# Kernel tuning notes

Measured on AMD Instinct MI355X. Metric: run time of the kernel, lower is better.

The kernel has to match this reference:

```python
import jax, jax.numpy as jnp
import numpy as np

B, S, E, H = 2, 2048, 1024, 16
DK = E // H


def setup_inputs() -> dict:
    key = jax.random.key(0)
    ks = jax.random.split(key, 11)
    std = 1.0 / np.sqrt(E)
    inp = {
        "q": jax.random.normal(ks[0], (B, S, E), jnp.float32),
        "k": jax.random.normal(ks[1], (B, S, E), jnp.float32),
        "v": jax.random.normal(ks[2], (B, S, E), jnp.float32),
        # causal mask, broadcast over batch and heads; scores with mask==0 get -1e9
        "mask": jnp.tril(jnp.ones((S, S), jnp.int32))[None, None],
        # torch nn.Linear weights: [out_features, in_features]
        "w_q": jax.random.normal(ks[3], (E, E), jnp.float32) * std,
        "b_q": jax.random.normal(ks[4], (E,), jnp.float32) * std,
        "w_k": jax.random.normal(ks[5], (E, E), jnp.float32) * std,
        "b_k": jax.random.normal(ks[6], (E,), jnp.float32) * std,
        "w_v": jax.random.normal(ks[7], (E, E), jnp.float32) * std,
        "b_v": jax.random.normal(ks[8], (E,), jnp.float32) * std,
        "w_o": jax.random.normal(ks[9], (E, E), jnp.float32) * std,
        "b_o": jax.random.normal(ks[10], (E,), jnp.float32) * std,
    }
    return inp


def reference(q, k, v, mask, w_q, b_q, w_k, b_k, w_v, b_v, w_o, b_o):
    # linear projections (torch Linear: x @ W.T + b)
    query = q @ w_q.T + b_q
    key = k @ w_k.T + b_k
    value = v @ w_v.T + b_v
    # [B, S, E] -> [B, H, S, DK]
    query = query.reshape(B, S, H, DK).transpose(0, 2, 1, 3)
    key = key.reshape(B, S, H, DK).transpose(0, 2, 1, 3)
    value = value.reshape(B, S, H, DK).transpose(0, 2, 1, 3)
    scale = 1.0 / jnp.sqrt(jnp.asarray(DK, query.dtype))
    scores = jnp.einsum("bhqd,bhkd->bhqk", query, key) * scale
    scores = jnp.where(mask == 0, jnp.asarray(-1e9, scores.dtype), scores)
    attn = jax.nn.softmax(scores, axis=-1)  # dropout p=0.0 -> identity
    x = jnp.einsum("bhqk,bhkd->bhqd", attn, value)
    x = x.transpose(0, 2, 1, 3).reshape(B, S, E)
    return x @ w_o.T + b_o
```

## Files before the change

kernel.cpp:

```cpp
#include <hip/hip_runtime.h>
#include <stdint.h>

typedef __attribute__((ext_vector_type(8))) short short8;
typedef __attribute__((ext_vector_type(4))) float f32x4;
typedef unsigned short u16;

#define SEQ 2048
#define EMB 1024
#define NH 16
#define DK 64
#define MTOT 4096
#define CEXP 0.18033688011112042f

__device__ __forceinline__ u16 f2bf(float f) {
  union { float f; unsigned int u; } x; x.f = f;
  unsigned int r = x.u + 0x7fffu + ((x.u >> 16) & 1u);
  return (u16)(r >> 16);
}

__device__ __forceinline__ void gload_lds16(const void* g, void* l) {
  __builtin_amdgcn_global_load_lds(
      (const __attribute__((address_space(1))) unsigned int*)g,
      (__attribute__((address_space(3))) unsigned int*)l,
      16, 0, 0);
}

__global__ __launch_bounds__(256) void cvt3(const float* __restrict__ a,
                                            const float* __restrict__ b,
                                            const float* __restrict__ c,
                                            u16* __restrict__ d) {
  const float* s = (blockIdx.y == 0) ? a : ((blockIdx.y == 1) ? b : c);
  size_t base = (size_t)blockIdx.y * (MTOT * (size_t)EMB / 4);
  int i = blockIdx.x * 256 + threadIdx.x;
  float4 v = ((const float4*)s)[i];
  ushort4 o;
  o.x = f2bf(v.x); o.y = f2bf(v.y); o.z = f2bf(v.z); o.w = f2bf(v.w);
  ((ushort4*)d)[base + i] = o;
}

__global__ __launch_bounds__(256) void cvt4(const float* __restrict__ a,
                                            const float* __restrict__ b,
                                            const float* __restrict__ c,
                                            const float* __restrict__ e,
                                            u16* __restrict__ d) {
  const float* s = (blockIdx.y == 0) ? a
                 : ((blockIdx.y == 1) ? b : ((blockIdx.y == 2) ? c : e));
  size_t base = (size_t)blockIdx.y * ((size_t)EMB * EMB / 4);
  int i = blockIdx.x * 256 + threadIdx.x;
  float4 v = ((const float4*)s)[i];
  ushort4 o;
  o.x = f2bf(v.x); o.y = f2bf(v.y); o.z = f2bf(v.z); o.w = f2bf(v.w);
  ((ushort4*)d)[base + i] = o;
}

template <int MODE>
__device__ __forceinline__ void gemm_core(const u16* __restrict__ A,
                                          const u16* __restrict__ W,
                                          const float* __restrict__ bias,
                                          void* __restrict__ dst,
                                          int m0, int n0,
                                          u16* As, u16* Bs) {
  const int K = EMB;
  int tid = threadIdx.x, lane = tid & 63, wid = tid >> 6;
  int g = lane >> 4, l15 = lane & 15;
  int wr = wid >> 1, wc = wid & 1;

  f32x4 acc[4][4];
#pragma unroll
  for (int mi = 0; mi < 4; ++mi)
#pragma unroll
    for (int ni = 0; ni < 4; ++ni) acc[mi][ni] = (f32x4)(0.0f);

  for (int kt = 0; kt < K / 64; ++kt) {
    int k0 = kt * 64;
#pragma unroll
    for (int i = 0; i < 4; ++i) {
      int off = (wid * 4 + i) * 1024;
      int elem = (off >> 1) + lane * 8;
      int row = elem >> 6, col = elem & 63;
      gload_lds16(A + (size_t)(m0 + row) * K + k0 + col, (char*)As + off);
      gload_lds16(W + (size_t)(n0 + row) * K + k0 + col, (char*)Bs + off);
    }
    __syncthreads();
#pragma unroll
    for (int kk = 0; kk < 2; ++kk) {
      short8 af[4], bf[4];
#pragma unroll
      for (int mi = 0; mi < 4; ++mi)
        af[mi] = *(const short8*)&As[(wr * 64 + mi * 16 + l15) * 64 + kk * 32 + 8 * g];
#pragma unroll
      for (int ni = 0; ni < 4; ++ni)
        bf[ni] = *(const short8*)&Bs[(wc * 64 + ni * 16 + l15) * 64 + kk * 32 + 8 * g];
#pragma unroll
      for (int mi = 0; mi < 4; ++mi)
#pragma unroll
        for (int ni = 0; ni < 4; ++ni)
          acc[mi][ni] = __builtin_amdgcn_mfma_f32_16x16x32_bf16(af[mi], bf[ni],
                                                                acc[mi][ni], 0, 0, 0);
    }
    __syncthreads();
  }

#pragma unroll
  for (int ni = 0; ni < 4; ++ni) {
    int n_g = n0 + wc * 64 + ni * 16 + l15;
    float bv = bias[n_g];
#pragma unroll
    for (int mi = 0; mi < 4; ++mi) {
#pragma unroll
      for (int j = 0; j < 4; ++j) {
        int m_g = m0 + wr * 64 + mi * 16 + 4 * g + j;
        float v = acc[mi][ni][j] + bv;
        if (MODE == 0) {
          int b = m_g >> 11, s = m_g & (SEQ - 1);
          int h = n_g >> 6, d = n_g & 63;
          ((u16*)dst)[((((size_t)b * NH + h) * SEQ + s) << 6) + d] = f2bf(v);
        } else {
          ((float*)dst)[(size_t)m_g * EMB + n_g] = v;
        }
      }
    }
  }
}

__global__ __launch_bounds__(256, 2) void gemm_qkv(const u16* __restrict__ Aall,
                                                   const u16* __restrict__ Wall,
                                                   const float* __restrict__ bq,
                                                   const float* __restrict__ bk,
                                                   const float* __restrict__ bv,
                                                   u16* __restrict__ QKVh) {
  __shared__ __align__(16) u16 As[128 * 64];
  __shared__ __align__(16) u16 Bs[128 * 64];
  int bl = blockIdx.x;
  int xcd = bl & 7, i = bl >> 3;
  int bx = i & 7;
  int j = i >> 3;
  int z = j >> 2;
  int by = xcd * 4 + (j & 3);
  const u16* A = Aall + (size_t)z * MTOT * EMB;
  const u16* W = Wall + (size_t)z * EMB * EMB;
  const float* bias = (z == 0) ? bq : ((z == 1) ? bk : bv);
  u16* dst = QKVh + (size_t)z * MTOT * EMB;
  gemm_core<0>(A, W, bias, dst, by * 128, bx * 128, As, Bs);
}

__global__ __launch_bounds__(256, 2) void gemm_out(const u16* __restrict__ X,
                                                   const u16* __restrict__ Wo,
                                                   const float* __restrict__ bo,
                                                   float* __restrict__ out) {
  __shared__ __align__(16) u16 As[128 * 64];
  __shared__ __align__(16) u16 Bs[128 * 64];
  int bl = blockIdx.x;
  int xcd = bl & 7, i = bl >> 3;
  int bx = i & 7;
  int by = xcd * 4 + (i >> 3);
  gemm_core<1>(X, Wo, bo, out, by * 128, bx * 128, As, Bs);
}

__global__ __launch_bounds__(256, 4) void flash_attn(const u16* __restrict__ Qh,
                                                     const u16* __restrict__ Kh,
                                                     const u16* __restrict__ Vh,
                                                     u16* __restrict__ X) {
  __shared__ __align__(16) u16 Ks[2][64][64];
  __shared__ __align__(16) u16 Vt[2][64][64];

  int tid = threadIdx.x, lane = tid & 63, wid = tid >> 6;
  int g = lane >> 4, l15 = lane & 15;

  int bl = blockIdx.x;
  int xcd = bl & 7, idx = bl >> 3;
  int c = idx & 31, r = idx >> 5;
  int bh = xcd * 4 + r;
  int cc = (r >= 2) ? ((c + 16) & 31) : c;
  int qt = (r & 1) ? (31 - cc) : cc;

  int q0 = qt * 64, qw = q0 + wid * 16;
  int qrow = qw + l15;

  const short8* qp = (const short8*)(Qh + ((size_t)bh * SEQ + qrow) * DK + 8 * g);
  short8 fq0 = qp[0], fq1 = qp[4];

  int kvbase = 8 * (l15 >> 2) + (l15 & 3);
  int ksw = ((l15 & 3) | (((l15 >> 2) & 1) << 2)) << 3;
  int vsw = (l15 & 7) << 3;
  const u16* Kb = Kh + (size_t)bh * SEQ * DK;
  const u16* Vb = Vh + (size_t)bh * SEQ * DK;

  int krow_st = wid * 16 + (lane >> 3);
  int kcol_st = (lane & 7) * 8;

  f32x4 sc[4], oacc[4];
#pragma unroll
  for (int i = 0; i < 4; ++i) oacc[i] = (f32x4)(0.0f);
  float m_run = -1e30f, l_part = 0.0f;

#pragma unroll
  for (int i = 0; i < 2; ++i) {
    int rw = krow_st + i * 8;
    int wsw = (((rw & 3) | (((rw >> 3) & 1) << 2)) << 3);
    short8 kt = *(const short8*)(Kb + (size_t)rw * DK + kcol_st);
    *(short8*)(&Ks[0][0][0] + rw * 64 + (kcol_st ^ wsw)) = kt;
  }
#pragma unroll
  for (int it2 = 0; it2 < 2; ++it2) {
    int kvb = wid * 8 + it2 * 32;
    short8 tmp;
#pragma unroll
    for (int i = 0; i < 8; ++i)
      tmp[i] = (short)Vb[(size_t)(kvb + i) * DK + lane];
    *(short8*)(&Vt[0][0][0] + lane * 64 + (kvb ^ ((lane & 7) << 3))) = tmp;
  }
  __syncthreads();

  for (int t = 0; t <= qt; ++t) {
    int kv0 = t * 64;
    int cur = t & 1;

    short8 ktmp[2];
    u16 vtmp[16];
    if (t < qt) {
      int kvn = kv0 + 64;
#pragma unroll
      for (int i = 0; i < 2; ++i)
        ktmp[i] = *(const short8*)(Kb + (size_t)(kvn + krow_st + i * 8) * DK + kcol_st);
#pragma unroll
      for (int it2 = 0; it2 < 2; ++it2)
#pragma unroll
        for (int i = 0; i < 8; ++i)
          vtmp[it2 * 8 + i] = Vb[(size_t)(kvn + wid * 8 + it2 * 32 + i) * DK + lane];
    }

    {
      const u16* base = &Ks[cur][0][0];
      short8 kf[4][2];
#pragma unroll
      for (int cq = 0; cq < 4; ++cq) {
        int krow = kvbase + 4 * (cq & 1) + 32 * (cq >> 1);
        kf[cq][0] = *(const short8*)(base + krow * 64 + ((8 * g) ^ ksw));
        kf[cq][1] = *(const short8*)(base + krow * 64 + ((8 * g + 32) ^ ksw));
      }
      __builtin_amdgcn_s_setprio(1);
#pragma unroll
      for (int cq = 0; cq < 4; ++cq) {
        f32x4 z = (f32x4)(0.0f);
        z = __builtin_amdgcn_mfma_f32_16x16x32_bf16(kf[cq][0], fq0, z, 0, 0, 0);
        z = __builtin_amdgcn_mfma_f32_16x16x32_bf16(kf[cq][1], fq1, z, 0, 0, 0);
        sc[cq] = z;
      }
      __builtin_amdgcn_s_setprio(0);
    }

    if (t == qt) {
#pragma unroll
      for (int cq = 0; cq < 4; ++cq) {
        int kvc = kv0 + 8 * g + 4 * (cq & 1) + 32 * (cq >> 1);
#pragma unroll
        for (int j = 0; j < 4; ++j)
          if (kvc + j > qrow) sc[cq][j] = -1e30f;
      }
    }

    float vmax = sc[0][0];
#pragma unroll
    for (int cq = 0; cq < 4; ++cq)
#pragma unroll
      for (int j = 0; j < 4; ++j) vmax = fmaxf(vmax, sc[cq][j]);
    vmax = fmaxf(vmax, __shfl_xor(vmax, 16));
    vmax = fmaxf(vmax, __shfl_xor(vmax, 32));

    if (!__all(vmax - m_run <= 44.0f)) {
      float mnew = fmaxf(m_run, vmax);
      float alpha = exp2f((m_run - mnew) * CEXP);
      l_part *= alpha;
#pragma unroll
      for (int c2 = 0; c2 < 4; ++c2)
#pragma unroll
        for (int j = 0; j < 4; ++j) oacc[c2][j] *= alpha;
      m_run = mnew;
    }

#pragma unroll
    for (int cq = 0; cq < 4; ++cq)
#pragma unroll
      for (int j = 0; j < 4; ++j) {
        float p = exp2f((sc[cq][j] - m_run) * CEXP);
        sc[cq][j] = p;
        l_part += p;
      }

    union { short8 s8; uint32_t w[4]; } pa[2];
#pragma unroll
    for (int h = 0; h < 2; ++h)
#pragma unroll
      for (int i = 0; i < 4; ++i) {
        float lo = sc[2 * h + (i >> 1)][(i & 1) * 2];
        float hi = sc[2 * h + (i >> 1)][(i & 1) * 2 + 1];
        asm("v_cvt_pk_bf16_f32 %0, %1, %2" : "=v"(pa[h].w[i]) : "v"(lo), "v"(hi));
      }

    __builtin_amdgcn_s_setprio(1);
#pragma unroll
    for (int c2 = 0; c2 < 4; ++c2)
#pragma unroll
      for (int h = 0; h < 2; ++h) {
        short8 av = *(const short8*)(&Vt[cur][0][0] + (c2 * 16 + l15) * 64 +
                                     ((h * 32 + 8 * g) ^ vsw));
        oacc[c2] = __builtin_amdgcn_mfma_f32_16x16x32_bf16(av, pa[h].s8,
                                                           oacc[c2], 0, 0, 0);
      }
    __builtin_amdgcn_s_setprio(0);

    if (t < qt) {
#pragma unroll
      for (int i = 0; i < 2; ++i) {
        int rw = krow_st + i * 8;
        int wsw = (((rw & 3) | (((rw >> 3) & 1) << 2)) << 3);
        *(short8*)(&Ks[cur ^ 1][0][0] + rw * 64 + (kcol_st ^ wsw)) = ktmp[i];
      }
#pragma unroll
      for (int it2 = 0; it2 < 2; ++it2) {
        short8 w;
#pragma unroll
        for (int i = 0; i < 8; ++i) w[i] = (short)vtmp[it2 * 8 + i];
        int kvb = wid * 8 + it2 * 32;
        *(short8*)(&Vt[cur ^ 1][0][0] + lane * 64 + (kvb ^ ((lane & 7) << 3))) = w;
      }
    }
    __syncthreads();
  }

  float ls = l_part;
  ls += __shfl_xor(ls, 16);
  ls += __shfl_xor(ls, 32);
  float inv = 1.0f / ls;
  u16* ow = &Vt[0][0][0] + wid * 16 * 64;
#pragma unroll
  for (int c2 = 0; c2 < 4; ++c2)
#pragma unroll
    for (int jp = 0; jp < 2; ++jp) {
      float lo = oacc[c2][2 * jp] * inv, hi = oacc[c2][2 * jp + 1] * inv;
      uint32_t w;
      asm("v_cvt_pk_bf16_f32 %0, %1, %2" : "=v"(w) : "v"(lo), "v"(hi));
      *(uint32_t*)&ow[l15 * 64 + c2 * 16 + 4 * g + 2 * jp] = w;
    }
  __syncthreads();
  int rr = lane >> 2, dc = (lane & 3) * 16;
  short8 o0 = *(const short8*)&ow[rr * 64 + dc];
  short8 o1 = *(const short8*)&ow[rr * 64 + dc + 8];
  int b = bh >> 4, hh = bh & 15;
  size_t xo = ((size_t)b * SEQ + qw + rr) * EMB + hh * 64 + dc;
  *(short8*)&X[xo] = o0;
  *(short8*)&X[xo + 8] = o1;
}

extern "C" void kernel_launch(void* const* d_in, const int* in_sizes, int n_in,
                              void* d_out, int out_size, void* d_ws, size_t ws_size,
                              hipStream_t stream) {
  const float* q  = (const float*)d_in[0];
  const float* k  = (const float*)d_in[1];
  const float* v  = (const float*)d_in[2];
  const float* wq = (const float*)d_in[4];
  const float* bq = (const float*)d_in[5];
  const float* wk = (const float*)d_in[6];
  const float* bk = (const float*)d_in[7];
  const float* wv = (const float*)d_in[8];
  const float* bv = (const float*)d_in[9];
  const float* wo = (const float*)d_in[10];
  const float* bo = (const float*)d_in[11];

  u16* Aall = (u16*)d_ws;
  u16* Wall = Aall + (size_t)3 * MTOT * EMB;
  u16* QKVh = Wall + (size_t)4 * EMB * EMB;
  u16* Xb   = QKVh + (size_t)3 * MTOT * EMB;

  cvt3<<<dim3(MTOT * EMB / 4 / 256, 3), 256, 0, stream>>>(q, k, v, Aall);
  cvt4<<<dim3(EMB * EMB / 4 / 256, 4), 256, 0, stream>>>(wq, wk, wv, wo, Wall);

  gemm_qkv<<<768, 256, 0, stream>>>(Aall, Wall, bq, bk, bv, QKVh);

  const u16* Qh = QKVh;
  const u16* Kh = QKVh + (size_t)MTOT * EMB;
  const u16* Vh = QKVh + (size_t)2 * MTOT * EMB;
  flash_attn<<<1024, 256, 0, stream>>>(Qh, Kh, Vh, Xb);

  gemm_out<<<256, 256, 0, stream>>>(Xb, Wall + (size_t)3 * EMB * EMB, bo, (float*)d_out);
}
```

Measured before the change: 125.9 us.

## Pair causal q-tiles per block and peel diagonal tile out of attention loop

```diff
diff --git a/kernel.cpp b/kernel.cpp
--- a/kernel.cpp
+++ b/kernel.cpp
@@ -169,16 +169,9 @@
 
   int bl = blockIdx.x;
   int xcd = bl & 7, idx = bl >> 3;
-  int c = idx & 31, r = idx >> 5;
-  int bh = xcd * 4 + r;
-  int cc = (r >= 2) ? ((c + 16) & 31) : c;
-  int qt = (r & 1) ? (31 - cc) : cc;
-
-  int q0 = qt * 64, qw = q0 + wid * 16;
-  int qrow = qw + l15;
-
-  const short8* qp = (const short8*)(Qh + ((size_t)bh * SEQ + qrow) * DK + 8 * g);
-  short8 fq0 = qp[0], fq1 = qp[4];
+  int bhl = idx >> 4;
+  int p = idx & 15;
+  int bh = xcd * 4 + bhl;
 
   int kvbase = 8 * (l15 >> 2) + (l15 & 3);
   int ksw = ((l15 & 3) | (((l15 >> 2) & 1) << 2)) << 3;
@@ -189,48 +182,152 @@
   int krow_st = wid * 16 + (lane >> 3);
   int kcol_st = (lane & 7) * 8;
 
-  f32x4 sc[4], oacc[4];
-#pragma unroll
-  for (int i = 0; i < 4; ++i) oacc[i] = (f32x4)(0.0f);
-  float m_run = -1e30f, l_part = 0.0f;
-
-#pragma unroll
-  for (int i = 0; i < 2; ++i) {
-    int rw = krow_st + i * 8;
-    int wsw = (((rw & 3) | (((rw >> 3) & 1) << 2)) << 3);
-    short8 kt = *(const short8*)(Kb + (size_t)rw * DK + kcol_st);
-    *(short8*)(&Ks[0][0][0] + rw * 64 + (kcol_st ^ wsw)) = kt;
-  }
-#pragma unroll
-  for (int it2 = 0; it2 < 2; ++it2) {
-    int kvb = wid * 8 + it2 * 32;
-    short8 tmp;
-#pragma unroll
-    for (int i = 0; i < 8; ++i)
-      tmp[i] = (short)Vb[(size_t)(kvb + i) * DK + lane];
-    *(short8*)(&Vt[0][0][0] + lane * 64 + (kvb ^ ((lane & 7) << 3))) = tmp;
-  }
-  __syncthreads();
-
-  for (int t = 0; t <= qt; ++t) {
-    int kv0 = t * 64;
-    int cur = t & 1;
-
-    short8 ktmp[2];
-    u16 vtmp[16];
-    if (t < qt) {
-      int kvn = kv0 + 64;
-#pragma unroll
-      for (int i = 0; i < 2; ++i)
-        ktmp[i] = *(const short8*)(Kb + (size_t)(kvn + krow_st + i * 8) * DK + kcol_st);
-#pragma unroll
-      for (int it2 = 0; it2 < 2; ++it2)
-#pragma unroll
-        for (int i = 0; i < 8; ++i)
-          vtmp[it2 * 8 + i] = Vb[(size_t)(kvn + wid * 8 + it2 * 32 + i) * DK + lane];
+  for (int half = 0; half < 2; ++half) {
+    int qt = half ? (31 - p) : p;
+    int qw = qt * 64 + wid * 16;
+    int qrow = qw + l15;
+
+    const short8* qp = (const short8*)(Qh + ((size_t)bh * SEQ + qrow) * DK + 8 * g);
+    short8 fq0 = qp[0], fq1 = qp[4];
+
+    f32x4 sc[4], oacc[4];
+#pragma unroll
+    for (int i = 0; i < 4; ++i) oacc[i] = (f32x4)(0.0f);
+    float m_run = -1e30f, l_part = 0.0f;
+
+    __syncthreads();
+
+#pragma unroll
+    for (int i = 0; i < 2; ++i) {
+      int rw = krow_st + i * 8;
+      int wsw = (((rw & 3) | (((rw >> 3) & 1) << 2)) << 3);
+      short8 kt = *(const short8*)(Kb + (size_t)rw * DK + kcol_st);
+      *(short8*)(&Ks[0][0][0] + rw * 64 + (kcol_st ^ wsw)) = kt;
+    }
+#pragma unroll
+    for (int it2 = 0; it2 < 2; ++it2) {
+      int kvb = wid * 8 + it2 * 32;
+      short8 tmp;
+#pragma unroll
+      for (int i = 0; i < 8; ++i)
+        tmp[i] = (short)Vb[(size_t)(kvb + i) * DK + lane];
+      *(short8*)(&Vt[0][0][0] + lane * 64 + (kvb ^ ((lane & 7) << 3))) = tmp;
+    }
+    __syncthreads();
+
+    for (int t = 0; t < qt; ++t) {
+      int kv0 = t * 64;
+      int cur = t & 1;
+
+      short8 ktmp[2];
+      u16 vtmp[16];
+      {
+        int kvn = kv0 + 64;
+#pragma unroll
+        for (int i = 0; i < 2; ++i)
+          ktmp[i] = *(const short8*)(Kb + (size_t)(kvn + krow_st + i * 8) * DK + kcol_st);
+#pragma unroll
+        for (int it2 = 0; it2 < 2; ++it2)
+#pragma unroll
+          for (int i = 0; i < 8; ++i)
+            vtmp[it2 * 8 + i] = Vb[(size_t)(kvn + wid * 8 + it2 * 32 + i) * DK + lane];
+      }
+
+      {
+        const u16* base = &Ks[cur][0][0];
+        short8 kf[4][2];
+#pragma unroll
+        for (int cq = 0; cq < 4; ++cq) {
+          int krow = kvbase + 4 * (cq & 1) + 32 * (cq >> 1);
+          kf[cq][0] = *(const short8*)(base + krow * 64 + ((8 * g) ^ ksw));
+          kf[cq][1] = *(const short8*)(base + krow * 64 + ((8 * g + 32) ^ ksw));
+        }
+        __builtin_amdgcn_s_setprio(1);
+#pragma unroll
+        for (int cq = 0; cq < 4; ++cq) {
+          f32x4 z = (f32x4)(0.0f);
+          z = __builtin_amdgcn_mfma_f32_16x16x32_bf16(kf[cq][0], fq0, z, 0, 0, 0);
+          z = __builtin_amdgcn_mfma_f32_16x16x32_bf16(kf[cq][1], fq1, z, 0, 0, 0);
+          sc[cq] = z;
+        }
+        __builtin_amdgcn_s_setprio(0);
+      }
+
+      float m01a = fmaxf(sc[0][0], sc[0][1]), m01b = fmaxf(sc[0][2], sc[0][3]);
+      float m23a = fmaxf(sc[1][0], sc[1][1]), m23b = fmaxf(sc[1][2], sc[1][3]);
+      float m45a = fmaxf(sc[2][0], sc[2][1]), m45b = fmaxf(sc[2][2], sc[2][3]);
+      float m67a = fmaxf(sc[3][0], sc[3][1]), m67b = fmaxf(sc[3][2], sc[3][3]);
+      float vmax = fmaxf(fmaxf(fmaxf(m01a, m01b), fmaxf(m23a, m23b)),
+                         fmaxf(fmaxf(m45a, m45b), fmaxf(m67a, m67b)));
+      vmax = fmaxf(vmax, __shfl_xor(vmax, 16));
+      vmax = fmaxf(vmax, __shfl_xor(vmax, 32));
+
+      if (!__all(vmax - m_run <= 44.0f)) {
+        float mnew = fmaxf(m_run, vmax);
+        float alpha = exp2f((m_run - mnew) * CEXP);
+        l_part *= alpha;
+#pragma unroll
+        for (int c2 = 0; c2 < 4; ++c2)
+#pragma unroll
+          for (int j = 0; j < 4; ++j) oacc[c2][j] *= alpha;
+        m_run = mnew;
+      }
+
+      float negm = -m_run * CEXP;
+      float ls0 = 0.f, ls1 = 0.f, ls2 = 0.f, ls3 = 0.f;
+#pragma unroll
+      for (int cq = 0; cq < 4; ++cq) {
+        float p0 = exp2f(fmaf(sc[cq][0], CEXP, negm));
+        float p1 = exp2f(fmaf(sc[cq][1], CEXP, negm));
+        float p2 = exp2f(fmaf(sc[cq][2], CEXP, negm));
+        float p3 = exp2f(fmaf(sc[cq][3], CEXP, negm));
+        sc[cq][0] = p0; sc[cq][1] = p1; sc[cq][2] = p2; sc[cq][3] = p3;
+        ls0 += p0; ls1 += p1; ls2 += p2; ls3 += p3;
+      }
+      l_part += (ls0 + ls1) + (ls2 + ls3);
+
+      union { short8 s8; uint32_t w[4]; } pa[2];
+#pragma unroll
+      for (int h = 0; h < 2; ++h)
+#pragma unroll
+        for (int i = 0; i < 4; ++i) {
+          float lo = sc[2 * h + (i >> 1)][(i & 1) * 2];
+          float hi = sc[2 * h + (i >> 1)][(i & 1) * 2 + 1];
+          asm("v_cvt_pk_bf16_f32 %0, %1, %2" : "=v"(pa[h].w[i]) : "v"(lo), "v"(hi));
+        }
+
+      __builtin_amdgcn_s_setprio(1);
+#pragma unroll
+      for (int c2 = 0; c2 < 4; ++c2)
+#pragma unroll
+        for (int h = 0; h < 2; ++h) {
+          short8 av = *(const short8*)(&Vt[cur][0][0] + (c2 * 16 + l15) * 64 +
+                                       ((h * 32 + 8 * g) ^ vsw));
+          oacc[c2] = __builtin_amdgcn_mfma_f32_16x16x32_bf16(av, pa[h].s8,
+                                                             oacc[c2], 0, 0, 0);
+        }
+      __builtin_amdgcn_s_setprio(0);
+
+#pragma unroll
+      for (int i = 0; i < 2; ++i) {
+        int rw = krow_st + i * 8;
+        int wsw = (((rw & 3) | (((rw >> 3) & 1) << 2)) << 3);
+        *(short8*)(&Ks[cur ^ 1][0][0] + rw * 64 + (kcol_st ^ wsw)) = ktmp[i];
+      }
+#pragma unroll
+      for (int it2 = 0; it2 < 2; ++it2) {
+        short8 w;
+#pragma unroll
+        for (int i = 0; i < 8; ++i) w[i] = (short)vtmp[it2 * 8 + i];
+        int kvb = wid * 8 + it2 * 32;
+        *(short8*)(&Vt[cur ^ 1][0][0] + lane * 64 + (kvb ^ ((lane & 7) << 3))) = w;
+      }
+      __syncthreads();
     }
 
     {
+      int kv0 = qt * 64;
+      int cur = qt & 1;
       const u16* base = &Ks[cur][0][0];
       short8 kf[4][2];
 #pragma unroll
@@ -248,9 +345,7 @@
         sc[cq] = z;
       }
       __builtin_amdgcn_s_setprio(0);
-    }
-
-    if (t == qt) {
+
 #pragma unroll
       for (int cq = 0; cq < 4; ++cq) {
         int kvc = kv0 + 8 * g + 4 * (cq & 1) + 32 * (cq >> 1);
@@ -258,99 +353,83 @@
         for (int j = 0; j < 4; ++j)
           if (kvc + j > qrow) sc[cq][j] = -1e30f;
       }
-    }
-
-    float vmax = sc[0][0];
-#pragma unroll
-    for (int cq = 0; cq < 4; ++cq)
-#pragma unroll
-      for (int j = 0; j < 4; ++j) vmax = fmaxf(vmax, sc[cq][j]);
-    vmax = fmaxf(vmax, __shfl_xor(vmax, 16));
-    vmax = fmaxf(vmax, __shfl_xor(vmax, 32));
-
-    if (!__all(vmax - m_run <= 44.0f)) {
-      float mnew = fmaxf(m_run, vmax);
-      float alpha = exp2f((m_run - mnew) * CEXP);
-      l_part *= alpha;
+
+      float vmax = sc[0][0];
+#pragma unroll
+      for (int cq = 0; cq < 4; ++cq)
+#pragma unroll
+        for (int j = 0; j < 4; ++j) vmax = fmaxf(vmax, sc[cq][j]);
+      vmax = fmaxf(vmax, __shfl_xor(vmax, 16));
+      vmax = fmaxf(vmax, __shfl_xor(vmax, 32));
+
+      if (!__all(vmax - m_run <= 44.0f)) {
+        float mnew = fmaxf(m_run, vmax);
+        float alpha = exp2f((m_run - mnew) * CEXP);
+        l_part *= alpha;
+#pragma unroll
+        for (int c2 = 0; c2 < 4; ++c2)
+#pragma unroll
+          for (int j = 0; j < 4; ++j) oacc[c2][j] *= alpha;
+        m_run = mnew;
+      }
+
+      float negm = -m_run * CEXP;
+#pragma unroll
+      for (int cq = 0; cq < 4; ++cq)
+#pragma unroll
+        for (int j = 0; j < 4; ++j) {
+          float pp = exp2f(fmaf(sc[cq][j], CEXP, negm));
+          sc[cq][j] = pp;
+          l_part += pp;
+        }
+
+      union { short8 s8; uint32_t w[4]; } pa[2];
+#pragma unroll
+      for (int h = 0; h < 2; ++h)
+#pragma unroll
+        for (int i = 0; i < 4; ++i) {
+          float lo = sc[2 * h + (i >> 1)][(i & 1) * 2];
+          float hi = sc[2 * h + (i >> 1)][(i & 1) * 2 + 1];
+          asm("v_cvt_pk_bf16_f32 %0, %1, %2" : "=v"(pa[h].w[i]) : "v"(lo), "v"(hi));
+        }
+
+      __builtin_amdgcn_s_setprio(1);
 #pragma unroll
       for (int c2 = 0; c2 < 4; ++c2)
 #pragma unroll
-        for (int j = 0; j < 4; ++j) oacc[c2][j] *= alpha;
-      m_run = mnew;
-    }
-
-#pragma unroll
-    for (int cq = 0; cq < 4; ++cq)
-#pragma unroll
-      for (int j = 0; j < 4; ++j) {
-        float p = exp2f((sc[cq][j] - m_run) * CEXP);
-        sc[cq][j] = p;
-        l_part += p;
-      }
-
-    union { short8 s8; uint32_t w[4]; } pa[2];
-#pragma unroll
-    for (int h = 0; h < 2; ++h)
-#pragma unroll
-      for (int i = 0; i < 4; ++i) {
-        float lo = sc[2 * h + (i >> 1)][(i & 1) * 2];
-        float hi = sc[2 * h + (i >> 1)][(i & 1) * 2 + 1];
-        asm("v_cvt_pk_bf16_f32 %0, %1, %2" : "=v"(pa[h].w[i]) : "v"(lo), "v"(hi));
-      }
-
-    __builtin_amdgcn_s_setprio(1);
+        for (int h = 0; h < 2; ++h) {
+          short8 av = *(const short8*)(&Vt[cur][0][0] + (c2 * 16 + l15) * 64 +
+                                       ((h * 32 + 8 * g) ^ vsw));
+          oacc[c2] = __builtin_amdgcn_mfma_f32_16x16x32_bf16(av, pa[h].s8,
+                                                             oacc[c2], 0, 0, 0);
+        }
+      __builtin_amdgcn_s_setprio(0);
+    }
+    __syncthreads();
+
+    float ls = l_part;
+    ls += __shfl_xor(ls, 16);
+    ls += __shfl_xor(ls, 32);
+    float inv = 1.0f / ls;
+    u16* ow = &Vt[0][0][0] + wid * 16 * 64;
 #pragma unroll
     for (int c2 = 0; c2 < 4; ++c2)
 #pragma unroll
-      for (int h = 0; h < 2; ++h) {
-        short8 av = *(const short8*)(&Vt[cur][0][0] + (c2 * 16 + l15) * 64 +
-                                     ((h * 32 + 8 * g) ^ vsw));
-        oacc[c2] = __builtin_amdgcn_mfma_f32_16x16x32_bf16(av, pa[h].s8,
-                                                           oacc[c2], 0, 0, 0);
-      }
-    __builtin_amdgcn_s_setprio(0);
-
-    if (t < qt) {
-#pragma unroll
-      for (int i = 0; i < 2; ++i) {
-        int rw = krow_st + i * 8;
-        int wsw = (((rw & 3) | (((rw >> 3) & 1) << 2)) << 3);
-        *(short8*)(&Ks[cur ^ 1][0][0] + rw * 64 + (kcol_st ^ wsw)) = ktmp[i];
-      }
-#pragma unroll
-      for (int it2 = 0; it2 < 2; ++it2) {
-        short8 w;
-#pragma unroll
-        for (int i = 0; i < 8; ++i) w[i] = (short)vtmp[it2 * 8 + i];
-        int kvb = wid * 8 + it2 * 32;
-        *(short8*)(&Vt[cur ^ 1][0][0] + lane * 64 + (kvb ^ ((lane & 7) << 3))) = w;
-      }
-    }
-    __syncthreads();
+      for (int jp = 0; jp < 2; ++jp) {
+        float lo = oacc[c2][2 * jp] * inv, hi = oacc[c2][2 * jp + 1] * inv;
+        uint32_t w;
+        asm("v_cvt_pk_bf16_f32 %0, %1, %2" : "=v"(w) : "v"(lo), "v"(hi));
+        *(uint32_t*)&ow[l15 * 64 + c2 * 16 + 4 * g + 2 * jp] = w;
+      }
+    __syncthreads();
+    int rr = lane >> 2, dc = (lane & 3) * 16;
+    short8 o0 = *(const short8*)&ow[rr * 64 + dc];
+    short8 o1 = *(const short8*)&ow[rr * 64 + dc + 8];
+    int b = bh >> 4, hh = bh & 15;
+    size_t xo = ((size_t)b * SEQ + qw + rr) * EMB + hh * 64 + dc;
+    *(short8*)&X[xo] = o0;
+    *(short8*)&X[xo + 8] = o1;
   }
-
-  float ls = l_part;
-  ls += __shfl_xor(ls, 16);
-  ls += __shfl_xor(ls, 32);
-  float inv = 1.0f / ls;
-  u16* ow = &Vt[0][0][0] + wid * 16 * 64;
-#pragma unroll
-  for (int c2 = 0; c2 < 4; ++c2)
-#pragma unroll
-    for (int jp = 0; jp < 2; ++jp) {
-      float lo = oacc[c2][2 * jp] * inv, hi = oacc[c2][2 * jp + 1] * inv;
-      uint32_t w;
-      asm("v_cvt_pk_bf16_f32 %0, %1, %2" : "=v"(w) : "v"(lo), "v"(hi));
-      *(uint32_t*)&ow[l15 * 64 + c2 * 16 + 4 * g + 2 * jp] = w;
-    }
-  __syncthreads();
-  int rr = lane >> 2, dc = (lane & 3) * 16;
-  short8 o0 = *(const short8*)&ow[rr * 64 + dc];
-  short8 o1 = *(const short8*)&ow[rr * 64 + dc + 8];
-  int b = bh >> 4, hh = bh & 15;
-  size_t xo = ((size_t)b * SEQ + qw + rr) * EMB + hh * 64 + dc;
-  *(short8*)&X[xo] = o0;
-  *(short8*)&X[xo + 8] = o1;
 }
 
 extern "C" void kernel_launch(void* const* d_in, const int* in_sizes, int n_in,
@@ -381,7 +460,7 @@
   const u16* Qh = QKVh;
   const u16* Kh = QKVh + (size_t)MTOT * EMB;
   const u16* Vh = QKVh + (size_t)2 * MTOT * EMB;
-  flash_attn<<<1024, 256, 0, stream>>>(Qh, Kh, Vh, Xb);
+  flash_attn<<<512, 256, 0, stream>>>(Qh, Kh, Vh, Xb);
 
   gemm_out<<<256, 256, 0, stream>>>(Xb, Wall + (size_t)3 * EMB * EMB, bo, (float*)d_out);
 }
```

Result: no change. 126.5 us (+0.5%).

## Widen flash-attention blocks to 128 query rows sharing K/V tiles

Applied to the files above, without the earlier changes.

```diff
diff --git a/kernel.cpp b/kernel.cpp
--- a/kernel.cpp
+++ b/kernel.cpp
@@ -157,7 +157,7 @@
   gemm_core<1>(X, Wo, bo, out, by * 128, bx * 128, As, Bs);
 }
 
-__global__ __launch_bounds__(256, 4) void flash_attn(const u16* __restrict__ Qh,
+__global__ __launch_bounds__(512, 4) void flash_attn(const u16* __restrict__ Qh,
                                                      const u16* __restrict__ Kh,
                                                      const u16* __restrict__ Vh,
                                                      u16* __restrict__ X) {
@@ -169,13 +169,14 @@
 
   int bl = blockIdx.x;
   int xcd = bl & 7, idx = bl >> 3;
-  int c = idx & 31, r = idx >> 5;
-  int bh = xcd * 4 + r;
-  int cc = (r >= 2) ? ((c + 16) & 31) : c;
-  int qt = (r & 1) ? (31 - cc) : cc;
-
-  int q0 = qt * 64, qw = q0 + wid * 16;
+  int bhl = idx & 3, u = idx >> 2;
+  int qb = (u < 8) ? u : 23 - u;
+  int bh = xcd * 4 + bhl;
+
+  int qw = qb * 128 + wid * 16;
   int qrow = qw + l15;
+  int td = 2 * qb + (wid >> 2);
+  int NT = 2 * qb + 2;
 
   const short8* qp = (const short8*)(Qh + ((size_t)bh * SEQ + qrow) * DK + 8 * g);
   short8 fq0 = qp[0], fq1 = qp[4];
@@ -186,7 +187,7 @@
   const u16* Kb = Kh + (size_t)bh * SEQ * DK;
   const u16* Vb = Vh + (size_t)bh * SEQ * DK;
 
-  int krow_st = wid * 16 + (lane >> 3);
+  int krow_st = wid * 8 + (lane >> 3);
   int kcol_st = (lane & 7) * 8;
 
   f32x4 sc[4], oacc[4];
@@ -194,137 +195,122 @@
   for (int i = 0; i < 4; ++i) oacc[i] = (f32x4)(0.0f);
   float m_run = -1e30f, l_part = 0.0f;
 
-#pragma unroll
-  for (int i = 0; i < 2; ++i) {
-    int rw = krow_st + i * 8;
-    int wsw = (((rw & 3) | (((rw >> 3) & 1) << 2)) << 3);
-    short8 kt = *(const short8*)(Kb + (size_t)rw * DK + kcol_st);
-    *(short8*)(&Ks[0][0][0] + rw * 64 + (kcol_st ^ wsw)) = kt;
-  }
-#pragma unroll
-  for (int it2 = 0; it2 < 2; ++it2) {
-    int kvb = wid * 8 + it2 * 32;
+  {
+    int wsw = (((krow_st & 3) | (((krow_st >> 3) & 1) << 2)) << 3);
+    short8 kt = *(const short8*)(Kb + (size_t)krow_st * DK + kcol_st);
+    *(short8*)(&Ks[0][0][0] + krow_st * 64 + (kcol_st ^ wsw)) = kt;
     short8 tmp;
 #pragma unroll
     for (int i = 0; i < 8; ++i)
-      tmp[i] = (short)Vb[(size_t)(kvb + i) * DK + lane];
-    *(short8*)(&Vt[0][0][0] + lane * 64 + (kvb ^ ((lane & 7) << 3))) = tmp;
+      tmp[i] = (short)Vb[(size_t)(wid * 8 + i) * DK + lane];
+    *(short8*)(&Vt[0][0][0] + lane * 64 + ((wid * 8) ^ ((lane & 7) << 3))) = tmp;
   }
   __syncthreads();
 
-  for (int t = 0; t <= qt; ++t) {
+  for (int t = 0; t < NT; ++t) {
     int kv0 = t * 64;
     int cur = t & 1;
 
-    short8 ktmp[2];
-    u16 vtmp[16];
-    if (t < qt) {
+    short8 ktmp;
+    u16 vtmp[8];
+    if (t < NT - 1) {
       int kvn = kv0 + 64;
-#pragma unroll
-      for (int i = 0; i < 2; ++i)
-        ktmp[i] = *(const short8*)(Kb + (size_t)(kvn + krow_st + i * 8) * DK + kcol_st);
-#pragma unroll
-      for (int it2 = 0; it2 < 2; ++it2)
-#pragma unroll
-        for (int i = 0; i < 8; ++i)
-          vtmp[it2 * 8 + i] = Vb[(size_t)(kvn + wid * 8 + it2 * 32 + i) * DK + lane];
-    }
-
-    {
-      const u16* base = &Ks[cur][0][0];
-      short8 kf[4][2];
-#pragma unroll
-      for (int cq = 0; cq < 4; ++cq) {
-        int krow = kvbase + 4 * (cq & 1) + 32 * (cq >> 1);
-        kf[cq][0] = *(const short8*)(base + krow * 64 + ((8 * g) ^ ksw));
-        kf[cq][1] = *(const short8*)(base + krow * 64 + ((8 * g + 32) ^ ksw));
+      ktmp = *(const short8*)(Kb + (size_t)(kvn + krow_st) * DK + kcol_st);
+#pragma unroll
+      for (int i = 0; i < 8; ++i)
+        vtmp[i] = Vb[(size_t)(kvn + wid * 8 + i) * DK + lane];
+    }
+
+    if (t <= td) {
+      {
+        const u16* base = &Ks[cur][0][0];
+        short8 kf[4][2];
+#pragma unroll
+        for (int cq = 0; cq < 4; ++cq) {
+          int krow = kvbase + 4 * (cq & 1) + 32 * (cq >> 1);
+          kf[cq][0] = *(const short8*)(base + krow * 64 + ((8 * g) ^ ksw));
+          kf[cq][1] = *(const short8*)(base + krow * 64 + ((8 * g + 32) ^ ksw));
+        }
+        __builtin_amdgcn_s_setprio(1);
+#pragma unroll
+        for (int cq = 0; cq < 4; ++cq) {
+          f32x4 z = (f32x4)(0.0f);
+          z = __builtin_amdgcn_mfma_f32_16x16x32_bf16(kf[cq][0], fq0, z, 0, 0, 0);
+          z = __builtin_amdgcn_mfma_f32_16x16x32_bf16(kf[cq][1], fq1, z, 0, 0, 0);
+          sc[cq] = z;
+        }
+        __builtin_amdgcn_s_setprio(0);
       }
+
+      if (t == td) {
+#pragma unroll
+        for (int cq = 0; cq < 4; ++cq) {
+          int kvc = kv0 + 8 * g + 4 * (cq & 1) + 32 * (cq >> 1);
+#pragma unroll
+          for (int j = 0; j < 4; ++j)
+            if (kvc + j > qrow) sc[cq][j] = -1e30f;
+        }
+      }
+
+      float vmax = sc[0][0];
+#pragma unroll
+      for (int cq = 0; cq < 4; ++cq)
+#pragma unroll
+        for (int j = 0; j < 4; ++j) vmax = fmaxf(vmax, sc[cq][j]);
+      vmax = fmaxf(vmax, __shfl_xor(vmax, 16));
+      vmax = fmaxf(vmax, __shfl_xor(vmax, 32));
+
+      if (!__all(vmax - m_run <= 44.0f)) {
+        float mnew = fmaxf(m_run, vmax);
+        float alpha = exp2f((m_run - mnew) * CEXP);
+        l_part *= alpha;
+#pragma unroll
+        for (int c2 = 0; c2 < 4; ++c2)
+#pragma unroll
+          for (int j = 0; j < 4; ++j) oacc[c2][j] *= alpha;
+        m_run = mnew;
+      }
+
+      float negm = -m_run * CEXP;
+#pragma unroll
+      for (int cq = 0; cq < 4; ++cq)
+#pragma unroll
+        for (int j = 0; j < 4; ++j) {
+          float p = exp2f(fmaf(sc[cq][j], CEXP, negm));
+          sc[cq][j] = p;
+          l_part += p;
+        }
+
+      union { short8 s8; uint32_t w[4]; } pa[2];
+#pragma unroll
+      for (int h = 0; h < 2; ++h)
+#pragma unroll
+        for (int i = 0; i < 4; ++i) {
+          float lo = sc[2 * h + (i >> 1)][(i & 1) * 2];
+          float hi = sc[2 * h + (i >> 1)][(i & 1) * 2 + 1];
+          asm("v_cvt_pk_bf16_f32 %0, %1, %2" : "=v"(pa[h].w[i]) : "v"(lo), "v"(hi));
+        }
+
       __builtin_amdgcn_s_setprio(1);
 #pragma unroll
-      for (int cq = 0; cq < 4; ++cq) {
-        f32x4 z = (f32x4)(0.0f);
-        z = __builtin_amdgcn_mfma_f32_16x16x32_bf16(kf[cq][0], fq0, z, 0, 0, 0);
-        z = __builtin_amdgcn_mfma_f32_16x16x32_bf16(kf[cq][1], fq1, z, 0, 0, 0);
-        sc[cq] = z;
-      }
+      for (int c2 = 0; c2 < 4; ++c2)
+#pragma unroll
+        for (int h = 0; h < 2; ++h) {
+          short8 av = *(const short8*)(&Vt[cur][0][0] + (c2 * 16 + l15) * 64 +
+                                       ((h * 32 + 8 * g) ^ vsw));
+          oacc[c2] = __builtin_amdgcn_mfma_f32_16x16x32_bf16(av, pa[h].s8,
+                                                             oacc[c2], 0, 0, 0);
+        }
       __builtin_amdgcn_s_setprio(0);
     }
 
-    if (t == qt) {
-#pragma unroll
-      for (int cq = 0; cq < 4; ++cq) {
-        int kvc = kv0 + 8 * g + 4 * (cq & 1) + 32 * (cq >> 1);
-#pragma unroll
-        for (int j = 0; j < 4; ++j)
-          if (kvc + j > qrow) sc[cq][j] = -1e30f;
-      }
-    }
-
-    float vmax = sc[0][0];
-#pragma unroll
-    for (int cq = 0; cq < 4; ++cq)
-#pragma unroll
-      for (int j = 0; j < 4; ++j) vmax = fmaxf(vmax, sc[cq][j]);
-    vmax = fmaxf(vmax, __shfl_xor(vmax, 16));
-    vmax = fmaxf(vmax, __shfl_xor(vmax, 32));
-
-    if (!__all(vmax - m_run <= 44.0f)) {
-      float mnew = fmaxf(m_run, vmax);
-      float alpha = exp2f((m_run - mnew) * CEXP);
-      l_part *= alpha;
-#pragma unroll
-      for (int c2 = 0; c2 < 4; ++c2)
-#pragma unroll
-        for (int j = 0; j < 4; ++j) oacc[c2][j] *= alpha;
-      m_run = mnew;
-    }
-
-#pragma unroll
-    for (int cq = 0; cq < 4; ++cq)
-#pragma unroll
-      for (int j = 0; j < 4; ++j) {
-        float p = exp2f((sc[cq][j] - m_run) * CEXP);
-        sc[cq][j] = p;
-        l_part += p;
-      }
-
-    union { short8 s8; uint32_t w[4]; } pa[2];
-#pragma unroll
-    for (int h = 0; h < 2; ++h)
-#pragma unroll
-      for (int i = 0; i < 4; ++i) {
-        float lo = sc[2 * h + (i >> 1)][(i & 1) * 2];
-        float hi = sc[2 * h + (i >> 1)][(i & 1) * 2 + 1];
-        asm("v_cvt_pk_bf16_f32 %0, %1, %2" : "=v"(pa[h].w[i]) : "v"(lo), "v"(hi));
-      }
-
-    __builtin_amdgcn_s_setprio(1);
-#pragma unroll
-    for (int c2 = 0; c2 < 4; ++c2)
-#pragma unroll
-      for (int h = 0; h < 2; ++h) {
-        short8 av = *(const short8*)(&Vt[cur][0][0] + (c2 * 16 + l15) * 64 +
-                                     ((h * 32 + 8 * g) ^ vsw));
-        oacc[c2] = __builtin_amdgcn_mfma_f32_16x16x32_bf16(av, pa[h].s8,
-                                                           oacc[c2], 0, 0, 0);
-      }
-    __builtin_amdgcn_s_setprio(0);
-
-    if (t < qt) {
-#pragma unroll
-      for (int i = 0; i < 2; ++i) {
-        int rw = krow_st + i * 8;
-        int wsw = (((rw & 3) | (((rw >> 3) & 1) << 2)) << 3);
-        *(short8*)(&Ks[cur ^ 1][0][0] + rw * 64 + (kcol_st ^ wsw)) = ktmp[i];
-      }
-#pragma unroll
-      for (int it2 = 0; it2 < 2; ++it2) {
-        short8 w;
-#pragma unroll
-        for (int i = 0; i < 8; ++i) w[i] = (short)vtmp[it2 * 8 + i];
-        int kvb = wid * 8 + it2 * 32;
-        *(short8*)(&Vt[cur ^ 1][0][0] + lane * 64 + (kvb ^ ((lane & 7) << 3))) = w;
-      }
+    if (t < NT - 1) {
+      int wsw = (((krow_st & 3) | (((krow_st >> 3) & 1) << 2)) << 3);
+      *(short8*)(&Ks[cur ^ 1][0][0] + krow_st * 64 + (kcol_st ^ wsw)) = ktmp;
+      short8 w;
+#pragma unroll
+      for (int i = 0; i < 8; ++i) w[i] = (short)vtmp[i];
+      *(short8*)(&Vt[cur ^ 1][0][0] + lane * 64 + ((wid * 8) ^ ((lane & 7) << 3))) = w;
     }
     __syncthreads();
   }
@@ -333,7 +319,7 @@
   ls += __shfl_xor(ls, 16);
   ls += __shfl_xor(ls, 32);
   float inv = 1.0f / ls;
-  u16* ow = &Vt[0][0][0] + wid * 16 * 64;
+  u16* ow = &Ks[0][0][0] + wid * 16 * 64;
 #pragma unroll
   for (int c2 = 0; c2 < 4; ++c2)
 #pragma unroll
@@ -381,7 +367,7 @@
   const u16* Qh = QKVh;
   const u16* Kh = QKVh + (size_t)MTOT * EMB;
   const u16* Vh = QKVh + (size_t)2 * MTOT * EMB;
-  flash_attn<<<1024, 256, 0, stream>>>(Qh, Kh, Vh, Xb);
+  flash_attn<<<512, 512, 0, stream>>>(Qh, Kh, Vh, Xb);
 
   gemm_out<<<256, 256, 0, stream>>>(Xb, Wall + (size_t)3 * EMB * EMB, bo, (float*)d_out);
 }
```

Result: slower. 130.1 us (+3.4%).

## Fuse fp32-to-bf16 activation conversion into QKV projection GEMM A-tile load

Applied to the files above, without the earlier changes.

```diff
diff --git a/kernel.cpp b/kernel.cpp
--- a/kernel.cpp
+++ b/kernel.cpp
@@ -25,24 +25,11 @@
       16, 0, 0);
 }
 
-__global__ __launch_bounds__(256) void cvt3(const float* __restrict__ a,
-                                            const float* __restrict__ b,
-                                            const float* __restrict__ c,
-                                            u16* __restrict__ d) {
-  const float* s = (blockIdx.y == 0) ? a : ((blockIdx.y == 1) ? b : c);
-  size_t base = (size_t)blockIdx.y * (MTOT * (size_t)EMB / 4);
-  int i = blockIdx.x * 256 + threadIdx.x;
-  float4 v = ((const float4*)s)[i];
-  ushort4 o;
-  o.x = f2bf(v.x); o.y = f2bf(v.y); o.z = f2bf(v.z); o.w = f2bf(v.w);
-  ((ushort4*)d)[base + i] = o;
-}
-
-__global__ __launch_bounds__(256) void cvt4(const float* __restrict__ a,
-                                            const float* __restrict__ b,
-                                            const float* __restrict__ c,
-                                            const float* __restrict__ e,
-                                            u16* __restrict__ d) {
+__global__ __launch_bounds__(256) void cvt_w(const float* __restrict__ a,
+                                             const float* __restrict__ b,
+                                             const float* __restrict__ c,
+                                             const float* __restrict__ e,
+                                             u16* __restrict__ d) {
   const float* s = (blockIdx.y == 0) ? a
                  : ((blockIdx.y == 1) ? b : ((blockIdx.y == 2) ? c : e));
   size_t base = (size_t)blockIdx.y * ((size_t)EMB * EMB / 4);
@@ -53,18 +40,37 @@
   ((ushort4*)d)[base + i] = o;
 }
 
-template <int MODE>
-__device__ __forceinline__ void gemm_core(const u16* __restrict__ A,
-                                          const u16* __restrict__ W,
-                                          const float* __restrict__ bias,
-                                          void* __restrict__ dst,
-                                          int m0, int n0,
-                                          u16* As, u16* Bs) {
+__global__ __launch_bounds__(256, 3) void gemm_qkv_f32(const float* __restrict__ qf,
+                                                       const float* __restrict__ kf,
+                                                       const float* __restrict__ vf,
+                                                       const u16* __restrict__ Wall,
+                                                       const float* __restrict__ bq,
+                                                       const float* __restrict__ bk,
+                                                       const float* __restrict__ bv,
+                                                       u16* __restrict__ QKVh) {
+  __shared__ __align__(16) u16 As[128 * 64];
+  __shared__ __align__(16) u16 Bs[128 * 64];
+
+  int bl = blockIdx.x;
+  int xcd = bl & 7, i0 = bl >> 3;
+  int bx = i0 & 7;
+  int j = i0 >> 3;
+  int z = j >> 2;
+  int by = xcd * 4 + (j & 3);
+  const float* A = (z == 0) ? qf : ((z == 1) ? kf : vf);
+  const u16* W = Wall + (size_t)z * EMB * EMB;
+  const float* bias = (z == 0) ? bq : ((z == 1) ? bk : bv);
+  u16* dst = QKVh + (size_t)z * MTOT * EMB;
+  int m0 = by * 128, n0 = bx * 128;
+
   const int K = EMB;
   int tid = threadIdx.x, lane = tid & 63, wid = tid >> 6;
   int g = lane >> 4, l15 = lane & 15;
   int wr = wid >> 1, wc = wid & 1;
 
+  int arow = tid >> 3;
+  int acol = (tid & 7) * 8;
+
   f32x4 acc[4][4];
 #pragma unroll
   for (int mi = 0; mi < 4; ++mi)
@@ -78,8 +84,20 @@
       int off = (wid * 4 + i) * 1024;
       int elem = (off >> 1) + lane * 8;
       int row = elem >> 6, col = elem & 63;
-      gload_lds16(A + (size_t)(m0 + row) * K + k0 + col, (char*)As + off);
       gload_lds16(W + (size_t)(n0 + row) * K + k0 + col, (char*)Bs + off);
+    }
+#pragma unroll
+    for (int it = 0; it < 4; ++it) {
+      int row = it * 32 + arow;
+      const float* ap = A + (size_t)(m0 + row) * K + k0 + acol;
+      float4 a0 = *(const float4*)ap;
+      float4 a1 = *(const float4*)(ap + 4);
+      union { short8 s8; uint32_t w[4]; } pk;
+      asm("v_cvt_pk_bf16_f32 %0, %1, %2" : "=v"(pk.w[0]) : "v"(a0.x), "v"(a0.y));
+      asm("v_cvt_pk_bf16_f32 %0, %1, %2" : "=v"(pk.w[1]) : "v"(a0.z), "v"(a0.w));
+      asm("v_cvt_pk_bf16_f32 %0, %1, %2" : "=v"(pk.w[2]) : "v"(a1.x), "v"(a1.y));
+      asm("v_cvt_pk_bf16_f32 %0, %1, %2" : "=v"(pk.w[3]) : "v"(a1.z), "v"(a1.w));
+      *(short8*)&As[it * 2048 + tid * 8] = pk.s8;
     }
     __syncthreads();
 #pragma unroll
@@ -104,57 +122,87 @@
 #pragma unroll
   for (int ni = 0; ni < 4; ++ni) {
     int n_g = n0 + wc * 64 + ni * 16 + l15;
-    float bv = bias[n_g];
+    float bv2 = bias[n_g];
 #pragma unroll
     for (int mi = 0; mi < 4; ++mi) {
 #pragma unroll
-      for (int j = 0; j < 4; ++j) {
-        int m_g = m0 + wr * 64 + mi * 16 + 4 * g + j;
-        float v = acc[mi][ni][j] + bv;
-        if (MODE == 0) {
-          int b = m_g >> 11, s = m_g & (SEQ - 1);
-          int h = n_g >> 6, d = n_g & 63;
-          ((u16*)dst)[((((size_t)b * NH + h) * SEQ + s) << 6) + d] = f2bf(v);
-        } else {
-          ((float*)dst)[(size_t)m_g * EMB + n_g] = v;
-        }
-      }
-    }
-  }
-}
-
-__global__ __launch_bounds__(256, 2) void gemm_qkv(const u16* __restrict__ Aall,
-                                                   const u16* __restrict__ Wall,
-                                                   const float* __restrict__ bq,
-                                                   const float* __restrict__ bk,
-                                                   const float* __restrict__ bv,
-                                                   u16* __restrict__ QKVh) {
-  __shared__ __align__(16) u16 As[128 * 64];
-  __shared__ __align__(16) u16 Bs[128 * 64];
-  int bl = blockIdx.x;
-  int xcd = bl & 7, i = bl >> 3;
-  int bx = i & 7;
-  int j = i >> 3;
-  int z = j >> 2;
-  int by = xcd * 4 + (j & 3);
-  const u16* A = Aall + (size_t)z * MTOT * EMB;
-  const u16* W = Wall + (size_t)z * EMB * EMB;
-  const float* bias = (z == 0) ? bq : ((z == 1) ? bk : bv);
-  u16* dst = QKVh + (size_t)z * MTOT * EMB;
-  gemm_core<0>(A, W, bias, dst, by * 128, bx * 128, As, Bs);
-}
-
-__global__ __launch_bounds__(256, 2) void gemm_out(const u16* __restrict__ X,
+      for (int j2 = 0; j2 < 4; ++j2) {
+        int m_g = m0 + wr * 64 + mi * 16 + 4 * g + j2;
+        float v = acc[mi][ni][j2] + bv2;
+        int b = m_g >> 11, s = m_g & (SEQ - 1);
+        int h = n_g >> 6, d = n_g & 63;
+        dst[((((size_t)b * NH + h) * SEQ + s) << 6) + d] = f2bf(v);
+      }
+    }
+  }
+}
+
+__global__ __launch_bounds__(256, 3) void gemm_out(const u16* __restrict__ X,
                                                    const u16* __restrict__ Wo,
                                                    const float* __restrict__ bo,
                                                    float* __restrict__ out) {
   __shared__ __align__(16) u16 As[128 * 64];
   __shared__ __align__(16) u16 Bs[128 * 64];
   int bl = blockIdx.x;
-  int xcd = bl & 7, i = bl >> 3;
-  int bx = i & 7;
-  int by = xcd * 4 + (i >> 3);
-  gemm_core<1>(X, Wo, bo, out, by * 128, bx * 128, As, Bs);
+  int xcd = bl & 7, i0 = bl >> 3;
+  int bx = i0 & 7;
+  int by = xcd * 4 + (i0 >> 3);
+  int m0 = by * 128, n0 = bx * 128;
+
+  const int K = EMB;
+  int tid = threadIdx.x, lane = tid & 63, wid = tid >> 6;
+  int g = lane >> 4, l15 = lane & 15;
+  int wr = wid >> 1, wc = wid & 1;
+
+  f32x4 acc[4][4];
+#pragma unroll
+  for (int mi = 0; mi < 4; ++mi)
+#pragma unroll
+    for (int ni = 0; ni < 4; ++ni) acc[mi][ni] = (f32x4)(0.0f);
+
+  for (int kt = 0; kt < K / 64; ++kt) {
+    int k0 = kt * 64;
+#pragma unroll
+    for (int i = 0; i < 4; ++i) {
+      int off = (wid * 4 + i) * 1024;
+      int elem = (off >> 1) + lane * 8;
+      int row = elem >> 6, col = elem & 63;
+      gload_lds16(X + (size_t)(m0 + row) * K + k0 + col, (char*)As + off);
+      gload_lds16(Wo + (size_t)(n0 + row) * K + k0 + col, (char*)Bs + off);
+    }
+    __syncthreads();
+#pragma unroll
+    for (int kk = 0; kk < 2; ++kk) {
+      short8 af[4], bf[4];
+#pragma unroll
+      for (int mi = 0; mi < 4; ++mi)
+        af[mi] = *(const short8*)&As[(wr * 64 + mi * 16 + l15) * 64 + kk * 32 + 8 * g];
+#pragma unroll
+      for (int ni = 0; ni < 4; ++ni)
+        bf[ni] = *(const short8*)&Bs[(wc * 64 + ni * 16 + l15) * 64 + kk * 32 + 8 * g];
+#pragma unroll
+      for (int mi = 0; mi < 4; ++mi)
+#pragma unroll
+        for (int ni = 0; ni < 4; ++ni)
+          acc[mi][ni] = __builtin_amdgcn_mfma_f32_16x16x32_bf16(af[mi], bf[ni],
+                                                                acc[mi][ni], 0, 0, 0);
+    }
+    __syncthreads();
+  }
+
+#pragma unroll
+  for (int ni = 0; ni < 4; ++ni) {
+    int n_g = n0 + wc * 64 + ni * 16 + l15;
+    float bv = bo[n_g];
+#pragma unroll
+    for (int mi = 0; mi < 4; ++mi) {
+#pragma unroll
+      for (int j = 0; j < 4; ++j) {
+        int m_g = m0 + wr * 64 + mi * 16 + 4 * g + j;
+        out[(size_t)m_g * EMB + n_g] = acc[mi][ni][j] + bv;
+      }
+    }
+  }
 }
 
 __global__ __launch_bounds__(256, 4) void flash_attn(const u16* __restrict__ Qh,
@@ -368,15 +416,13 @@
   const float* wo = (const float*)d_in[10];
   const float* bo = (const float*)d_in[11];
 
-  u16* Aall = (u16*)d_ws;
-  u16* Wall = Aall + (size_t)3 * MTOT * EMB;
+  u16* Wall = (u16*)d_ws;
   u16* QKVh = Wall + (size_t)4 * EMB * EMB;
   u16* Xb   = QKVh + (size_t)3 * MTOT * EMB;
 
-  cvt3<<<dim3(MTOT * EMB / 4 / 256, 3), 256, 0, stream>>>(q, k, v, Aall);
-  cvt4<<<dim3(EMB * EMB / 4 / 256, 4), 256, 0, stream>>>(wq, wk, wv, wo, Wall);
-
-  gemm_qkv<<<768, 256, 0, stream>>>(Aall, Wall, bq, bk, bv, QKVh);
+  cvt_w<<<dim3(EMB * EMB / 4 / 256, 4), 256, 0, stream>>>(wq, wk, wv, wo, Wall);
+
+  gemm_qkv_f32<<<768, 256, 0, stream>>>(q, k, v, Wall, bq, bk, bv, QKVh);
 
   const u16* Qh = QKVh;
   const u16* Kh = QKVh + (size_t)MTOT * EMB;
```

Result: no change. 128.2 us (+1.8%).
